# Kernel tuning notes

Hardware: AMD Instinct MI355X
Metric: run time of the kernel (lower is better)

Reference implementation:

```python
import jax, jax.numpy as jnp
import numpy as np


def gcn_layer(x, src, dst, deg_inv_sqrt, W, b):
    # PyG GCNConv: h = X W; out[i] = sum_{j->i} norm(j,i) * h[j] + deg_i^{-1} * h[i] + b
    n = x.shape[0]
    h = x @ W                                   # [N, out]
    norm = deg_inv_sqrt[src] * deg_inv_sqrt[dst]  # [E]
    msg = h[src] * norm[:, None]                # [E, out]
    agg = jax.ops.segment_sum(msg, dst, num_segments=n)
    # self-loop contribution (added loops with norm = deg_i^{-1})
    agg = agg + h * (deg_inv_sqrt * deg_inv_sqrt)[:, None]
    return agg + b


def setup_inputs() -> dict:
    key = jax.random.key(0)
    k1, k2, k3, k4, k5, k6 = jax.random.split(key, 6)
    N, E, IN, HID, OUT = 50000, 800000, 128, 128, 64
    x = jax.random.normal(k1, (N, IN), dtype=jnp.float32)
    edge_index = jax.random.randint(k2, (2, E), 0, N, dtype=jnp.int64)
    # glorot-ish init for weights, zeros-ish bias
    W1 = jax.random.normal(k3, (IN, HID), dtype=jnp.float32) * (1.0 / np.sqrt(IN))
    b1 = jax.random.normal(k4, (HID,), dtype=jnp.float32) * 0.01
    W2 = jax.random.normal(k5, (HID, OUT), dtype=jnp.float32) * (1.0 / np.sqrt(HID))
    b2 = jax.random.normal(k6, (OUT,), dtype=jnp.float32) * 0.01
    return {"x": x, "edge_index": edge_index, "W1": W1, "b1": b1, "W2": W2, "b2": b2}


def reference(x, edge_index, W1, b1, W2, b2):
    n = x.shape[0]
    src, dst = edge_index[0], edge_index[1]
    # degree with self-loops (PyG computes degree on the dst/col index)
    deg = jax.ops.segment_sum(jnp.ones_like(dst, dtype=x.dtype), dst, num_segments=n) + 1.0
    deg_inv_sqrt = jax.lax.rsqrt(deg)
    h = gcn_layer(x, src, dst, deg_inv_sqrt, W1, b1)
    h = jax.nn.relu(h)
    # F.dropout with training=False is identity (module evaluated in eval mode)
    out = gcn_layer(h, src, dst, deg_inv_sqrt, W2, b2)
    return out
```

## Files before the change

kernel.cpp:

```cpp
#include <hip/hip_runtime.h>
#include <stdint.h>

typedef __attribute__((ext_vector_type(8))) short short8;
typedef __attribute__((ext_vector_type(4))) float floatx4;

static inline size_t align256(size_t x) { return (x + 255) & ~size_t(255); }

__device__ __forceinline__ unsigned short f2bf(float f) {
    unsigned u = __float_as_uint(f);
    u += 0x7fff + ((u >> 16) & 1);
    return (unsigned short)(u >> 16);
}
__device__ __forceinline__ unsigned pack_bf16(float a, float b) {
    return (unsigned)f2bf(a) | ((unsigned)f2bf(b) << 16);
}
__device__ __forceinline__ float bf_lo(unsigned u) { return __uint_as_float(u << 16); }
__device__ __forceinline__ float bf_hi(unsigned u) { return __uint_as_float(u & 0xffff0000u); }

#define BSHIFT 7
#define NBMAX 1024
#define CH 2048
#define SCAP 3072

__device__ __forceinline__ bool detect_i32(const void* eidx, int E, int t) {
    const long long* e64 = (const long long*)eidx;
    int nchk = E < 256 ? E : 256;
    long long v = e64[t % nchk];
    int bad = (v < 0 || v > 0x7fffffffLL) ? 1 : 0;
    return __syncthreads_or(bad) != 0;
}

__global__ __launch_bounds__(256) void k_hist(const void* __restrict__ eidx, int E,
        int* __restrict__ chist, int NB, int NC,
        const float* __restrict__ W1, const float* __restrict__ W2,
        unsigned short* __restrict__ w1t, unsigned short* __restrict__ w2t,
        int K1, int M1, int K2, int M2) {
    __shared__ int hist[NBMAX];
    const int t = threadIdx.x, B = blockIdx.x;
    if (B < NC) {
        const int e0 = B * CH;
        const int e1 = (e0 + CH < E) ? e0 + CH : E;
        const bool i32 = detect_i32(eidx, E, t);
        const int* e32 = (const int*)eidx;
        const long long* e64 = (const long long*)eidx;
        for (int b0 = 0; b0 < NB; b0 += NBMAX) {
            int bw = (NB - b0 < NBMAX) ? NB - b0 : NBMAX;
            for (int i = t; i < bw; i += 256) hist[i] = 0;
            __syncthreads();
            for (int e = e0 + t; e < e1; e += 256) {
                int d = i32 ? e32[(size_t)E + e] : (int)e64[(size_t)E + e];
                int b = (d >> BSHIFT) - b0;
                if (b >= 0 && b < bw) atomicAdd(&hist[b], 1);
            }
            __syncthreads();
            for (int i = t; i < bw; i += 256) chist[(size_t)(b0 + i) * NC + B] = hist[i];
            __syncthreads();
        }
    } else if (B == NC) {
        for (int j = t; j < K1 * M1; j += 256) {
            int k = j / M1, n = j % M1;
            w1t[(size_t)n * K1 + k] = f2bf(W1[j]);
        }
    } else if (B == NC + 1) {
        for (int j = t; j < K2 * M2; j += 256) {
            int k = j / M2, n = j % M2;
            w2t[(size_t)n * K2 + k] = f2bf(W2[j]);
        }
    }
}

__global__ __launch_bounds__(256) void k_btot(const int* __restrict__ chist,
                                              int* __restrict__ btot, int NB, int NC) {
    int b = blockIdx.x * 4 + (threadIdx.x >> 6);
    if (b >= NB) return;
    int lane = threadIdx.x & 63;
    const int* row = chist + (size_t)b * NC;
    int v = 0;
    for (int i = lane; i < NC; i += 64) v += row[i];
    #pragma unroll
    for (int off = 32; off >= 1; off >>= 1) v += __shfl_xor(v, off, 64);
    if (lane == 0) btot[b] = v;
}

__global__ __launch_bounds__(1024) void k_bscan(const int* __restrict__ btot,
                                                int* __restrict__ bbase,
                                                int* __restrict__ rs_final,
                                                int NB, int N) {
    __shared__ int swt[16];
    const int t = threadIdx.x, lane = t & 63, w = t >> 6;
    int carry = 0;
    for (int base = 0; base < NB; base += 1024) {
        int i = base + t;
        int v = (i < NB) ? btot[i] : 0;
        int incl = v;
        #pragma unroll
        for (int off = 1; off < 64; off <<= 1) {
            int nbr = __shfl_up(incl, off, 64);
            if (lane >= off) incl += nbr;
        }
        if (lane == 63) swt[w] = incl;
        __syncthreads();
        int woff = 0;
        for (int j = 0; j < w; ++j) woff += swt[j];
        if (i < NB) bbase[i] = carry + woff + incl - v;
        int tot = 0;
        for (int j = 0; j < 16; ++j) tot += swt[j];
        carry += tot;
        __syncthreads();
    }
    if (t == 0) { bbase[NB] = carry; rs_final[N] = carry; }
}

__global__ __launch_bounds__(256) void k_hscan2(int* __restrict__ chist,
                                                const int* __restrict__ bbase,
                                                int NB, int NC) {
    int b = blockIdx.x * 4 + (threadIdx.x >> 6);
    if (b >= NB) return;
    int lane = threadIdx.x & 63;
    int* row = chist + (size_t)b * NC;
    int carry = bbase[b];
    for (int base = 0; base < NC; base += 64) {
        int i = base + lane;
        int v = (i < NC) ? row[i] : 0;
        int incl = v;
        #pragma unroll
        for (int off = 1; off < 64; off <<= 1) {
            int nbr = __shfl_up(incl, off, 64);
            if (lane >= off) incl += nbr;
        }
        if (i < NC) row[i] = carry + incl - v;
        carry += __shfl(incl, 63, 64);
    }
}

__global__ __launch_bounds__(256) void k_bfill(const void* __restrict__ eidx, int E,
                                               const int* __restrict__ chist,
                                               unsigned* __restrict__ bbuf, int NB, int NC) {
    __shared__ int rank[NBMAX];
    __shared__ int base[NBMAX];
    const int t = threadIdx.x, c = blockIdx.x;
    const int e0 = c * CH;
    const int e1 = (e0 + CH < E) ? e0 + CH : E;
    const bool i32 = detect_i32(eidx, E, t);
    const int* e32 = (const int*)eidx;
    const long long* e64 = (const long long*)eidx;
    for (int b0 = 0; b0 < NB; b0 += NBMAX) {
        int bw = (NB - b0 < NBMAX) ? NB - b0 : NBMAX;
        for (int i = t; i < bw; i += 256) {
            rank[i] = 0;
            base[i] = chist[(size_t)(b0 + i) * NC + c];
        }
        __syncthreads();
        for (int e = e0 + t; e < e1; e += 256) {
            int s, d;
            if (i32) { s = e32[e]; d = e32[(size_t)E + e]; }
            else     { s = (int)e64[e]; d = (int)e64[(size_t)E + e]; }
            int b = (d >> BSHIFT) - b0;
            if (b >= 0 && b < bw) {
                int slot = base[b] + atomicAdd(&rank[b], 1);
                bbuf[slot] = ((unsigned)(d & 127) << 25) | (unsigned)s;
            }
        }
        __syncthreads();
    }
}

__global__ __launch_bounds__(256) void k_sort(const unsigned* __restrict__ bbuf,
                                              const int* __restrict__ bbase,
                                              int* __restrict__ rs_final,
                                              float* __restrict__ dinv,
                                              int* __restrict__ esrc, int N) {
    __shared__ int hist[128];
    __shared__ int off[128];
    __shared__ int srcbuf[SCAP];
    const int b = blockIdx.x, t = threadIdx.x;
    const int node0 = b << BSHIFT;
    const int nloc = (N - node0 < 128) ? N - node0 : 128;
    const int s0 = bbase[b], s1 = bbase[b + 1];
    const int cnt = s1 - s0;
    if (t < 128) hist[t] = 0;
    __syncthreads();
    for (int i = s0 + t; i < s1; i += 256)
        atomicAdd(&hist[bbuf[i] >> 25], 1);
    __syncthreads();
    if (t < 64) {
        int carry = 0;
        #pragma unroll
        for (int base = 0; base < 128; base += 64) {
            int v = hist[base + t];
            int incl = v;
            #pragma unroll
            for (int o = 1; o < 64; o <<= 1) {
                int nbr = __shfl_up(incl, o, 64);
                if (t >= o) incl += nbr;
            }
            off[base + t] = carry + incl - v;
            carry += __shfl(incl, 63, 64);
        }
    }
    __syncthreads();
    if (t < nloc) {
        rs_final[node0 + t] = s0 + off[t];
        dinv[node0 + t] = rsqrtf((float)hist[t] + 1.0f);
    }
    __syncthreads();
    if (t < 128) hist[t] = 0;
    __syncthreads();
    if (cnt <= SCAP) {
        for (int i = s0 + t; i < s1; i += 256) {
            unsigned sd = bbuf[i];
            int lo = sd >> 25;
            int r = atomicAdd(&hist[lo], 1);
            srcbuf[off[lo] + r] = (int)(sd & 0x1ffffffu);
        }
        __syncthreads();
        for (int i = t; i < cnt; i += 256) esrc[s0 + i] = srcbuf[i];
    } else {
        for (int i = s0 + t; i < s1; i += 256) {
            unsigned sd = bbuf[i];
            int lo = sd >> 25;
            int r = atomicAdd(&hist[lo], 1);
            esrc[s0 + off[lo] + r] = (int)(sd & 0x1ffffffu);
        }
    }
}

template<int BN, bool AF32>
__global__ __launch_bounds__(256, 3) void k_gemm(
        const void* __restrict__ Av, const unsigned short* __restrict__ Bt,
        const float* __restrict__ dinv, unsigned short* __restrict__ C,
        int N, int M) {
    constexpr int LD = 136;
    __shared__ unsigned short As[64 * LD];
    __shared__ unsigned short Bs[BN * LD];
    const int tid = threadIdx.x;
    const int wave = tid >> 6, lane = tid & 63;
    const int q = lane >> 4, tm = lane & 15;
    const int row0 = blockIdx.x * 64;

    {
        const uint4* Bg = (const uint4*)Bt;
        #pragma unroll
        for (int it = 0; it < BN / 16; ++it) {
            int i = tid + it * 256;
            int r = i >> 4, o = i & 15;
            *(uint4*)&Bs[r * LD + o * 8] = Bg[(size_t)r * 16 + o];
        }
    }
    if (AF32) {
        const float4* Ag = (const float4*)Av;
        #pragma unroll
        for (int it = 0; it < 8; ++it) {
            int i = tid + it * 256;
            int r = i >> 5, o = i & 31;
            int row = row0 + r;
            float4 v = make_float4(0.f, 0.f, 0.f, 0.f);
            if (row < N) v = Ag[(size_t)row * 32 + o];
            uint2 pk;
            pk.x = pack_bf16(v.x, v.y);
            pk.y = pack_bf16(v.z, v.w);
            *(uint2*)&As[r * LD + o * 4] = pk;
        }
    } else {
        const uint4* Ag = (const uint4*)Av;
        #pragma unroll
        for (int it = 0; it < 4; ++it) {
            int i = tid + it * 256;
            int r = i >> 4, o = i & 15;
            int row = row0 + r;
            uint4 v = make_uint4(0, 0, 0, 0);
            if (row < N) v = Ag[(size_t)row * 16 + o];
            *(uint4*)&As[r * LD + o * 8] = v;
        }
    }
    __syncthreads();

    constexpr int NG = BN / 16;
    floatx4 acc[NG];
    #pragma unroll
    for (int g = 0; g < NG; ++g) acc[g] = (floatx4){0.f, 0.f, 0.f, 0.f};

    const int arow = wave * 16 + tm;
    #pragma unroll
    for (int kc = 0; kc < 4; ++kc) {
        short8 af = *(const short8*)&As[arow * LD + kc * 32 + q * 8];
        #pragma unroll
        for (int g = 0; g < NG; ++g) {
            short8 bf = *(const short8*)&Bs[(g * 16 + tm) * LD + kc * 32 + q * 8];
            acc[g] = __builtin_amdgcn_mfma_f32_16x16x32_bf16(af, bf, acc[g], 0, 0, 0);
        }
    }

    float dv[4];
    #pragma unroll
    for (int r = 0; r < 4; ++r) {
        int row = row0 + wave * 16 + q * 4 + r;
        dv[r] = (row < N) ? dinv[row] : 0.f;
    }
    #pragma unroll
    for (int g = 0; g < NG; ++g) {
        #pragma unroll
        for (int r = 0; r < 4; ++r) {
            int row = row0 + wave * 16 + q * 4 + r;
            if (row < N) C[(size_t)row * M + g * 16 + tm] = f2bf(dv[r] * acc[g][r]);
        }
    }
}

#define ACC8(v) do { \
    a0 += bf_lo((v).x); a1 += bf_hi((v).x); \
    a2 += bf_lo((v).y); a3 += bf_hi((v).y); \
    a4 += bf_lo((v).z); a5 += bf_hi((v).z); \
    a6 += bf_lo((v).w); a7 += bf_hi((v).w); } while (0)

__global__ __launch_bounds__(256) void k_agg128(const uint4* __restrict__ H4,
        const float* __restrict__ dinv, const int* __restrict__ rs,
        const int* __restrict__ esrc, const float* __restrict__ bias,
        uint4* __restrict__ out, int N) {
    int wid = (blockIdx.x * 256 + threadIdx.x) >> 6;
    if (wid >= N) return;
    int l = threadIdx.x & 63;
    int g = l >> 4;
    int q = l & 15;
    float a0 = 0.f, a1 = 0.f, a2 = 0.f, a3 = 0.f;
    float a4 = 0.f, a5 = 0.f, a6 = 0.f, a7 = 0.f;
    int k0 = rs[wid], kend = rs[wid + 1];
    for (int base = k0; base < kend; base += 64) {
        int rem = kend - base; if (rem > 64) rem = 64;
        int idx = esrc[base + (l < rem ? l : 0)];
        int e0 = 0;
        for (; e0 + 16 <= rem; e0 += 16) {
            int s0 = __shfl(idx, e0 + g, 64);
            int s1 = __shfl(idx, e0 + 4 + g, 64);
            int s2 = __shfl(idx, e0 + 8 + g, 64);
            int s3 = __shfl(idx, e0 + 12 + g, 64);
            uint4 v0 = H4[(size_t)s0 * 16 + q];
            uint4 v1 = H4[(size_t)s1 * 16 + q];
            uint4 v2 = H4[(size_t)s2 * 16 + q];
            uint4 v3 = H4[(size_t)s3 * 16 + q];
            ACC8(v0); ACC8(v1); ACC8(v2); ACC8(v3);
        }
        for (; e0 + 4 <= rem; e0 += 4) {
            int s0 = __shfl(idx, e0 + g, 64);
            uint4 v0 = H4[(size_t)s0 * 16 + q];
            ACC8(v0);
        }
        if (e0 < rem) {
            int s0 = __shfl(idx, e0 + g, 64);
            if (e0 + g < rem) {
                uint4 v0 = H4[(size_t)s0 * 16 + q];
                ACC8(v0);
            }
        }
    }
    a0 += __shfl_xor(a0, 16, 64); a1 += __shfl_xor(a1, 16, 64);
    a2 += __shfl_xor(a2, 16, 64); a3 += __shfl_xor(a3, 16, 64);
    a4 += __shfl_xor(a4, 16, 64); a5 += __shfl_xor(a5, 16, 64);
    a6 += __shfl_xor(a6, 16, 64); a7 += __shfl_xor(a7, 16, 64);
    a0 += __shfl_xor(a0, 32, 64); a1 += __shfl_xor(a1, 32, 64);
    a2 += __shfl_xor(a2, 32, 64); a3 += __shfl_xor(a3, 32, 64);
    a4 += __shfl_xor(a4, 32, 64); a5 += __shfl_xor(a5, 32, 64);
    a6 += __shfl_xor(a6, 32, 64); a7 += __shfl_xor(a7, 32, 64);
    if (g == 0) {
        uint4 sv = H4[(size_t)wid * 16 + q];
        ACC8(sv);
        float di = dinv[wid];
        float4 bA = ((const float4*)bias)[q * 2];
        float4 bB = ((const float4*)bias)[q * 2 + 1];
        float o0 = fmaxf(fmaf(di, a0, bA.x), 0.f);
        float o1 = fmaxf(fmaf(di, a1, bA.y), 0.f);
        float o2 = fmaxf(fmaf(di, a2, bA.z), 0.f);
        float o3 = fmaxf(fmaf(di, a3, bA.w), 0.f);
        float o4 = fmaxf(fmaf(di, a4, bB.x), 0.f);
        float o5 = fmaxf(fmaf(di, a5, bB.y), 0.f);
        float o6 = fmaxf(fmaf(di, a6, bB.z), 0.f);
        float o7 = fmaxf(fmaf(di, a7, bB.w), 0.f);
        uint4 pk;
        pk.x = pack_bf16(o0, o1);
        pk.y = pack_bf16(o2, o3);
        pk.z = pack_bf16(o4, o5);
        pk.w = pack_bf16(o6, o7);
        out[(size_t)wid * 16 + q] = pk;
    }
}

__global__ __launch_bounds__(256) void k_agg64(const uint4* __restrict__ H4,
        const float* __restrict__ dinv, const int* __restrict__ rs,
        const int* __restrict__ esrc, const float* __restrict__ bias,
        float4* __restrict__ out, int N) {
    int wid = (blockIdx.x * 256 + threadIdx.x) >> 6;
    if (wid >= N) return;
    int l = threadIdx.x & 63;
    int g = l >> 3;
    int q = l & 7;
    float a0 = 0.f, a1 = 0.f, a2 = 0.f, a3 = 0.f;
    float a4 = 0.f, a5 = 0.f, a6 = 0.f, a7 = 0.f;
    int k0 = rs[wid], kend = rs[wid + 1];
    for (int base = k0; base < kend; base += 64) {
        int rem = kend - base; if (rem > 64) rem = 64;
        int idx = esrc[base + (l < rem ? l : 0)];
        int e0 = 0;
        for (; e0 + 32 <= rem; e0 += 32) {
            int s0 = __shfl(idx, e0 + g, 64);
            int s1 = __shfl(idx, e0 + 8 + g, 64);
            int s2 = __shfl(idx, e0 + 16 + g, 64);
            int s3 = __shfl(idx, e0 + 24 + g, 64);
            uint4 v0 = H4[(size_t)s0 * 8 + q];
            uint4 v1 = H4[(size_t)s1 * 8 + q];
            uint4 v2 = H4[(size_t)s2 * 8 + q];
            uint4 v3 = H4[(size_t)s3 * 8 + q];
            ACC8(v0); ACC8(v1); ACC8(v2); ACC8(v3);
        }
        for (; e0 + 8 <= rem; e0 += 8) {
            int s0 = __shfl(idx, e0 + g, 64);
            uint4 v0 = H4[(size_t)s0 * 8 + q];
            ACC8(v0);
        }
        if (e0 < rem) {
            int s0 = __shfl(idx, e0 + g, 64);
            if (e0 + g < rem) {
                uint4 v0 = H4[(size_t)s0 * 8 + q];
                ACC8(v0);
            }
        }
    }
    a0 += __shfl_xor(a0, 8, 64);  a1 += __shfl_xor(a1, 8, 64);
    a2 += __shfl_xor(a2, 8, 64);  a3 += __shfl_xor(a3, 8, 64);
    a4 += __shfl_xor(a4, 8, 64);  a5 += __shfl_xor(a5, 8, 64);
    a6 += __shfl_xor(a6, 8, 64);  a7 += __shfl_xor(a7, 8, 64);
    a0 += __shfl_xor(a0, 16, 64); a1 += __shfl_xor(a1, 16, 64);
    a2 += __shfl_xor(a2, 16, 64); a3 += __shfl_xor(a3, 16, 64);
    a4 += __shfl_xor(a4, 16, 64); a5 += __shfl_xor(a5, 16, 64);
    a6 += __shfl_xor(a6, 16, 64); a7 += __shfl_xor(a7, 16, 64);
    a0 += __shfl_xor(a0, 32, 64); a1 += __shfl_xor(a1, 32, 64);
    a2 += __shfl_xor(a2, 32, 64); a3 += __shfl_xor(a3, 32, 64);
    a4 += __shfl_xor(a4, 32, 64); a5 += __shfl_xor(a5, 32, 64);
    a6 += __shfl_xor(a6, 32, 64); a7 += __shfl_xor(a7, 32, 64);
    if (g == 0) {
        uint4 sv = H4[(size_t)wid * 8 + q];
        ACC8(sv);
        float di = dinv[wid];
        float4 bA = ((const float4*)bias)[q * 2];
        float4 bB = ((const float4*)bias)[q * 2 + 1];
        float4 oA, oB;
        oA.x = fmaf(di, a0, bA.x);
        oA.y = fmaf(di, a1, bA.y);
        oA.z = fmaf(di, a2, bA.z);
        oA.w = fmaf(di, a3, bA.w);
        oB.x = fmaf(di, a4, bB.x);
        oB.y = fmaf(di, a5, bB.y);
        oB.z = fmaf(di, a6, bB.z);
        oB.w = fmaf(di, a7, bB.w);
        out[(size_t)wid * 16 + q * 2]     = oA;
        out[(size_t)wid * 16 + q * 2 + 1] = oB;
    }
}

extern "C" void kernel_launch(void* const* d_in, const int* in_sizes, int n_in,
                              void* d_out, int out_size, void* d_ws, size_t ws_size,
                              hipStream_t stream) {
    const float* x  = (const float*)d_in[0];
    const void*  ei = d_in[1];
    const float* W1 = (const float*)d_in[2];
    const float* b1 = (const float*)d_in[3];
    const float* W2 = (const float*)d_in[4];
    const float* b2 = (const float*)d_in[5];

    int HID = in_sizes[3];
    int IN  = in_sizes[2] / HID;
    int OUT = in_sizes[4] / HID;
    int N   = in_sizes[0] / IN;
    int E   = in_sizes[1] / 2;
    int NB  = (N + 127) >> BSHIFT;
    int NC  = (E + CH - 1) / CH;

    char* p = (char*)d_ws;
    int* chist     = (int*)p;   p += align256((size_t)NB * NC * 4);
    int* btot      = (int*)p;   p += align256((size_t)NB * 4);
    int* bbase     = (int*)p;   p += align256((size_t)(NB + 1) * 4);
    int* rs_final  = (int*)p;   p += align256((size_t)(N + 1) * 4);
    int* esrc      = (int*)p;   p += align256((size_t)E * 4);
    float* dinv    = (float*)p; p += align256((size_t)N * 4);
    unsigned short* w1t = (unsigned short*)p; p += align256((size_t)HID * IN * 2);
    unsigned short* w2t = (unsigned short*)p; p += align256((size_t)OUT * HID * 2);
    size_t hb_bytes = (size_t)N * HID * 2, bbuf_bytes = (size_t)E * 4;
    unsigned* bbuf = (unsigned*)p;
    unsigned short* hb = (unsigned short*)p;
    p += align256(hb_bytes > bbuf_bytes ? hb_bytes : bbuf_bytes);
    unsigned short* h1b = (unsigned short*)p; p += align256((size_t)N * HID * 2);
    unsigned short* h2b = (unsigned short*)p; p += align256((size_t)N * OUT * 2);

    k_hist<<<NC + 2, 256, 0, stream>>>(ei, E, chist, NB, NC,
                                       W1, W2, w1t, w2t, IN, HID, HID, OUT);
    k_btot<<<(NB + 3) / 4, 256, 0, stream>>>(chist, btot, NB, NC);
    k_bscan<<<1, 1024, 0, stream>>>(btot, bbase, rs_final, NB, N);
    k_hscan2<<<(NB + 3) / 4, 256, 0, stream>>>(chist, bbase, NB, NC);
    k_bfill<<<NC, 256, 0, stream>>>(ei, E, chist, bbuf, NB, NC);
    k_sort<<<NB, 256, 0, stream>>>(bbuf, bbase, rs_final, dinv, esrc, N);

    k_gemm<128, true><<<(N + 63) / 64, 256, 0, stream>>>(x, w1t, dinv, hb, N, HID);
    k_agg128<<<(N + 3) / 4, 256, 0, stream>>>((const uint4*)hb, dinv, rs_final, esrc,
                                              b1, (uint4*)h1b, N);

    k_gemm<64, false><<<(N + 63) / 64, 256, 0, stream>>>(h1b, w2t, dinv, h2b, N, OUT);
    k_agg64<<<(N + 3) / 4, 256, 0, stream>>>((const uint4*)h2b, dinv, rs_final, esrc,
                                             b2, (float4*)d_out, N);
}
```

Measured before the change: 201.4 us.

## Sort edges within each destination by source-range bucket for gather locality

The per-block counting sort now keys on destination-low bits combined with 6 bits of source index (a 13-bit key, 8192 bins), so edges for each destination are grouped by coarse source range. The aim is better cache locality in the later gather of h[src] during aggregation. In exchange the sort kernel zeroes and scans a 32KB shared histogram per block, which raises its own cost and shared-memory footprint and may reduce occupancy.

```diff
diff --git a/kernel.cpp b/kernel.cpp
--- a/kernel.cpp
+++ b/kernel.cpp
@@ -21,6 +21,7 @@
 #define NBMAX 1024
 #define CH 2048
 #define SCAP 3072
+#define KB 8192
 
 __device__ __forceinline__ bool detect_i32(const void* eidx, int E, int t) {
     const long long* e64 = (const long long*)eidx;
@@ -28,6 +29,24 @@
     long long v = e64[t % nchk];
     int bad = (v < 0 || v > 0x7fffffffLL) ? 1 : 0;
     return __syncthreads_or(bad) != 0;
+}
+
+__device__ __forceinline__ int blockScanExcl(int v, int t, int* sw, int* tot) {
+    int lane = t & 63, w = t >> 6;
+    int incl = v;
+    #pragma unroll
+    for (int off = 1; off < 64; off <<= 1) {
+        int nbr = __shfl_up(incl, off, 64);
+        if (lane >= off) incl += nbr;
+    }
+    if (lane == 63) sw[w] = incl;
+    __syncthreads();
+    int woff = 0;
+    for (int j = 0; j < w; ++j) woff += sw[j];
+    int tt = sw[0] + sw[1] + sw[2] + sw[3];
+    __syncthreads();
+    *tot = tt;
+    return woff + incl - v;
 }
 
 __global__ __launch_bounds__(256) void k_hist(const void* __restrict__ eidx, int E,
@@ -165,62 +184,68 @@
     }
 }
 
-__global__ __launch_bounds__(256) void k_sort(const unsigned* __restrict__ bbuf,
-                                              const int* __restrict__ bbase,
-                                              int* __restrict__ rs_final,
-                                              float* __restrict__ dinv,
-                                              int* __restrict__ esrc, int N) {
-    __shared__ int hist[128];
-    __shared__ int off[128];
+__global__ __launch_bounds__(256, 3) void k_sort(const unsigned* __restrict__ bbuf,
+                                                 const int* __restrict__ bbase,
+                                                 int* __restrict__ rs_final,
+                                                 float* __restrict__ dinv,
+                                                 int* __restrict__ esrc, int N) {
+    __shared__ int h13[KB];
     __shared__ int srcbuf[SCAP];
+    __shared__ int sw[4];
     const int b = blockIdx.x, t = threadIdx.x;
     const int node0 = b << BSHIFT;
     const int nloc = (N - node0 < 128) ? N - node0 : 128;
     const int s0 = bbase[b], s1 = bbase[b + 1];
     const int cnt = s1 - s0;
-    if (t < 128) hist[t] = 0;
-    __syncthreads();
-    for (int i = s0 + t; i < s1; i += 256)
-        atomicAdd(&hist[bbuf[i] >> 25], 1);
-    __syncthreads();
-    if (t < 64) {
-        int carry = 0;
-        #pragma unroll
-        for (int base = 0; base < 128; base += 64) {
-            int v = hist[base + t];
-            int incl = v;
-            #pragma unroll
-            for (int o = 1; o < 64; o <<= 1) {
-                int nbr = __shfl_up(incl, o, 64);
-                if (t >= o) incl += nbr;
-            }
-            off[base + t] = carry + incl - v;
-            carry += __shfl(incl, 63, 64);
+    #pragma unroll
+    for (int j = 0; j < KB / 256; ++j) h13[t + j * 256] = 0;
+    __syncthreads();
+    for (int i = s0 + t; i < s1; i += 256) {
+        unsigned u = bbuf[i];
+        unsigned src = u & 0x1ffffffu;
+        int key = (int)((u >> 25) << 6) | (int)((src >> 11) & 63u);
+        atomicAdd(&h13[key], 1);
+    }
+    __syncthreads();
+    {
+        const int CPT = KB / 256;
+        int s = 0;
+        #pragma unroll
+        for (int j = 0; j < CPT; ++j) s += h13[t * CPT + j];
+        int tot;
+        int run = blockScanExcl(s, t, sw, &tot);
+        #pragma unroll
+        for (int j = 0; j < CPT; ++j) {
+            int v = h13[t * CPT + j];
+            h13[t * CPT + j] = run;
+            run += v;
         }
     }
     __syncthreads();
     if (t < nloc) {
-        rs_final[node0 + t] = s0 + off[t];
-        dinv[node0 + t] = rsqrtf((float)hist[t] + 1.0f);
-    }
-    __syncthreads();
-    if (t < 128) hist[t] = 0;
+        int st = h13[t << 6];
+        int en = (t < 127) ? h13[(t + 1) << 6] : cnt;
+        rs_final[node0 + t] = s0 + st;
+        dinv[node0 + t] = rsqrtf((float)(en - st) + 1.0f);
+    }
     __syncthreads();
     if (cnt <= SCAP) {
         for (int i = s0 + t; i < s1; i += 256) {
-            unsigned sd = bbuf[i];
-            int lo = sd >> 25;
-            int r = atomicAdd(&hist[lo], 1);
-            srcbuf[off[lo] + r] = (int)(sd & 0x1ffffffu);
+            unsigned u = bbuf[i];
+            unsigned src = u & 0x1ffffffu;
+            int key = (int)((u >> 25) << 6) | (int)((src >> 11) & 63u);
+            int slot = atomicAdd(&h13[key], 1);
+            srcbuf[slot] = (int)src;
         }
         __syncthreads();
         for (int i = t; i < cnt; i += 256) esrc[s0 + i] = srcbuf[i];
     } else {
         for (int i = s0 + t; i < s1; i += 256) {
-            unsigned sd = bbuf[i];
-            int lo = sd >> 25;
-            int r = atomicAdd(&hist[lo], 1);
-            esrc[s0 + off[lo] + r] = (int)(sd & 0x1ffffffu);
+            unsigned u = bbuf[i];
+            unsigned src = u & 0x1ffffffu;
+            int key = (int)((u >> 25) << 6) | (int)((src >> 11) & 63u);
+            int slot = atomicAdd(&h13[key], 1);
+            esrc[s0 + slot] = (int)src;
         }
     }
 }
```

After: 205.7 us. 2.1% more time.

## Replace per-chunk histogram scans with global atomic cursors in bucket fill

Applied to the files above, without the earlier changes.

The bucketing pipeline drops the per-chunk column histogram and its two-level scan. A single scan kernel now sums a small fixed-chunk histogram to get bucket bases and cursors. Fill blocks recount their own edges and reserve slots with one global atomicAdd per bucket. This removes two kernel launches and a large chist matrix, at the cost of reading dst twice in bk_fill, making edge order within a bucket nondeterministic, and assuming NB fits in shared memory (NBMAX).

```diff
diff --git a/kernel.cpp b/kernel.cpp
--- a/kernel.cpp
+++ b/kernel.cpp
@@ -19,7 +19,8 @@
 
 #define BSHIFT 7
 #define NBMAX 1024
-#define CH 2048
+#define NHC 64
+#define NCF 128
 #define SCAP 3072
 
 __device__ __forceinline__ bool detect_i32(const void* eidx, int E, int t) {
@@ -31,37 +32,33 @@
 }
 
 __global__ __launch_bounds__(256) void k_hist(const void* __restrict__ eidx, int E,
-        int* __restrict__ chist, int NB, int NC,
+        int* __restrict__ chist, int NB,
         const float* __restrict__ W1, const float* __restrict__ W2,
         unsigned short* __restrict__ w1t, unsigned short* __restrict__ w2t,
         int K1, int M1, int K2, int M2) {
     __shared__ int hist[NBMAX];
     const int t = threadIdx.x, B = blockIdx.x;
-    if (B < NC) {
-        const int e0 = B * CH;
-        const int e1 = (e0 + CH < E) ? e0 + CH : E;
+    if (B < NHC) {
+        const int ehc = (E + NHC - 1) / NHC;
+        const int e0 = B * ehc;
+        const int e1 = (e0 + ehc < E) ? e0 + ehc : E;
         const bool i32 = detect_i32(eidx, E, t);
         const int* e32 = (const int*)eidx;
         const long long* e64 = (const long long*)eidx;
-        for (int b0 = 0; b0 < NB; b0 += NBMAX) {
-            int bw = (NB - b0 < NBMAX) ? NB - b0 : NBMAX;
-            for (int i = t; i < bw; i += 256) hist[i] = 0;
-            __syncthreads();
-            for (int e = e0 + t; e < e1; e += 256) {
-                int d = i32 ? e32[(size_t)E + e] : (int)e64[(size_t)E + e];
-                int b = (d >> BSHIFT) - b0;
-                if (b >= 0 && b < bw) atomicAdd(&hist[b], 1);
-            }
-            __syncthreads();
-            for (int i = t; i < bw; i += 256) chist[(size_t)(b0 + i) * NC + B] = hist[i];
-            __syncthreads();
-        }
-    } else if (B == NC) {
+        for (int i = t; i < NB; i += 256) hist[i] = 0;
+        __syncthreads();
+        for (int e = e0 + t; e < e1; e += 256) {
+            int d = i32 ? e32[(size_t)E + e] : (int)e64[(size_t)E + e];
+            atomicAdd(&hist[d >> BSHIFT], 1);
+        }
+        __syncthreads();
+        for (int i = t; i < NB; i += 256) chist[(size_t)i * NHC + B] = hist[i];
+    } else if (B == NHC) {
         for (int j = t; j < K1 * M1; j += 256) {
             int k = j / M1, n = j % M1;
             w1t[(size_t)n * K1 + k] = f2bf(W1[j]);
         }
-    } else if (B == NC + 1) {
+    } else if (B == NHC + 1) {
         for (int j = t; j < K2 * M2; j += 256) {
             int k = j / M2, n = j % M2;
             w2t[(size_t)n * K2 + k] = f2bf(W2[j]);
@@ -69,29 +66,23 @@
     }
 }
 
-__global__ __launch_bounds__(256) void k_btot(const int* __restrict__ chist,
-                                              int* __restrict__ btot, int NB, int NC) {
-    int b = blockIdx.x * 4 + (threadIdx.x >> 6);
-    if (b >= NB) return;
-    int lane = threadIdx.x & 63;
-    const int* row = chist + (size_t)b * NC;
-    int v = 0;
-    for (int i = lane; i < NC; i += 64) v += row[i];
-    #pragma unroll
-    for (int off = 32; off >= 1; off >>= 1) v += __shfl_xor(v, off, 64);
-    if (lane == 0) btot[b] = v;
-}
-
-__global__ __launch_bounds__(1024) void k_bscan(const int* __restrict__ btot,
-                                                int* __restrict__ bbase,
-                                                int* __restrict__ rs_final,
-                                                int NB, int N) {
+__global__ __launch_bounds__(1024) void k_scan1(const int* __restrict__ chist,
+        int* __restrict__ bbase, int* __restrict__ cursor,
+        int* __restrict__ rs_final, int NB, int N) {
     __shared__ int swt[16];
     const int t = threadIdx.x, lane = t & 63, w = t >> 6;
     int carry = 0;
     for (int base = 0; base < NB; base += 1024) {
         int i = base + t;
-        int v = (i < NB) ? btot[i] : 0;
+        int v = 0;
+        if (i < NB) {
+            const int4* row = (const int4*)(chist + (size_t)i * NHC);
+            #pragma unroll
+            for (int c = 0; c < NHC / 4; ++c) {
+                int4 q = row[c];
+                v += q.x + q.y + q.z + q.w;
+            }
+        }
         int incl = v;
         #pragma unroll
         for (int off = 1; off < 64; off <<= 1) {
@@ -102,7 +93,11 @@
         __syncthreads();
         int woff = 0;
         for (int j = 0; j < w; ++j) woff += swt[j];
-        if (i < NB) bbase[i] = carry + woff + incl - v;
+        if (i < NB) {
+            int ex = carry + woff + incl - v;
+            bbase[i] = ex;
+            cursor[i] = ex;
+        }
         int tot = 0;
         for (int j = 0; j < 16; ++j) tot += swt[j];
         carry += tot;
@@ -111,57 +106,39 @@
     if (t == 0) { bbase[NB] = carry; rs_final[N] = carry; }
 }
 
-__global__ __launch_bounds__(256) void k_hscan2(int* __restrict__ chist,
-                                                const int* __restrict__ bbase,
-                                                int NB, int NC) {
-    int b = blockIdx.x * 4 + (threadIdx.x >> 6);
-    if (b >= NB) return;
-    int lane = threadIdx.x & 63;
-    int* row = chist + (size_t)b * NC;
-    int carry = bbase[b];
-    for (int base = 0; base < NC; base += 64) {
-        int i = base + lane;
-        int v = (i < NC) ? row[i] : 0;
-        int incl = v;
-        #pragma unroll
-        for (int off = 1; off < 64; off <<= 1) {
-            int nbr = __shfl_up(incl, off, 64);
-            if (lane >= off) incl += nbr;
-        }
-        if (i < NC) row[i] = carry + incl - v;
-        carry += __shfl(incl, 63, 64);
-    }
-}
-
 __global__ __launch_bounds__(256) void k_bfill(const void* __restrict__ eidx, int E,
-                                               const int* __restrict__ chist,
-                                               unsigned* __restrict__ bbuf, int NB, int NC) {
+                                               int* __restrict__ cursor,
+                                               unsigned* __restrict__ bbuf, int NB) {
     __shared__ int rank[NBMAX];
     __shared__ int base[NBMAX];
-    const int t = threadIdx.x, c = blockIdx.x;
-    const int e0 = c * CH;
-    const int e1 = (e0 + CH < E) ? e0 + CH : E;
+    const int t = threadIdx.x, B = blockIdx.x;
+    const int ecf = (E + NCF - 1) / NCF;
+    const int e0 = B * ecf;
+    const int e1 = (e0 + ecf < E) ? e0 + ecf : E;
     const bool i32 = detect_i32(eidx, E, t);
     const int* e32 = (const int*)eidx;
     const long long* e64 = (const long long*)eidx;
-    for (int b0 = 0; b0 < NB; b0 += NBMAX) {
-        int bw = (NB - b0 < NBMAX) ? NB - b0 : NBMAX;
-        for (int i = t; i < bw; i += 256) {
-            rank[i] = 0;
-            base[i] = chist[(size_t)(b0 + i) * NC + c];
-        }
-        __syncthreads();
-        for (int e = e0 + t; e < e1; e += 256) {
-            int s, d;
-            if (i32) { s = e32[e]; d = e32[(size_t)E + e]; }
-            else     { s = (int)e64[e]; d = (int)e64[(size_t)E + e]; }
-            int b = (d >> BSHIFT) - b0;
-            if (b >= 0 && b < bw) {
-                int slot = base[b] + atomicAdd(&rank[b], 1);
-                bbuf[slot] = ((unsigned)(d & 127) << 25) | (unsigned)s;
-            }
-        }
-        __syncthreads();
+    for (int i = t; i < NB; i += 256) rank[i] = 0;
+    __syncthreads();
+    for (int e = e0 + t; e < e1; e += 256) {
+        int d = i32 ? e32[(size_t)E + e] : (int)e64[(size_t)E + e];
+        atomicAdd(&rank[d >> BSHIFT], 1);
+    }
+    __syncthreads();
+    for (int i = t; i < NB; i += 256) {
+        int c = rank[i];
+        base[i] = c ? atomicAdd(&cursor[i], c) : 0;
+    }
+    __syncthreads();
+    for (int i = t; i < NB; i += 256) rank[i] = 0;
+    __syncthreads();
+    for (int e = e0 + t; e < e1; e += 256) {
+        int s, d;
+        if (i32) { s = e32[e]; d = e32[(size_t)E + e]; }
+        else     { s = (int)e64[e]; d = (int)e64[(size_t)E + e]; }
+        int b = d >> BSHIFT;
+        int slot = base[b] + atomicAdd(&rank[b], 1);
+        bbuf[slot] = ((unsigned)(d & 127) << 25) | (unsigned)s;
     }
 }
 
@@ -472,12 +449,11 @@
     int N   = in_sizes[0] / IN;
     int E   = in_sizes[1] / 2;
     int NB  = (N + 127) >> BSHIFT;
-    int NC  = (E + CH - 1) / CH;
 
     char* p = (char*)d_ws;
-    int* chist     = (int*)p;   p += align256((size_t)NB * NC * 4);
-    int* btot      = (int*)p;   p += align256((size_t)NB * 4);
+    int* chist     = (int*)p;   p += align256((size_t)NB * NHC * 4);
     int* bbase     = (int*)p;   p += align256((size_t)(NB + 1) * 4);
+    int* cursor    = (int*)p;   p += align256((size_t)NB * 4);
     int* rs_final  = (int*)p;   p += align256((size_t)(N + 1) * 4);
     int* esrc      = (int*)p;   p += align256((size_t)E * 4);
     float* dinv    = (float*)p; p += align256((size_t)N * 4);
@@ -490,12 +466,10 @@
     unsigned short* h1b = (unsigned short*)p; p += align256((size_t)N * HID * 2);
     unsigned short* h2b = (unsigned short*)p; p += align256((size_t)N * OUT * 2);
 
-    k_hist<<<NC + 2, 256, 0, stream>>>(ei, E, chist, NB, NC,
-                                       W1, W2, w1t, w2t, IN, HID, HID, OUT);
-    k_btot<<<(NB + 3) / 4, 256, 0, stream>>>(chist, btot, NB, NC);
-    k_bscan<<<1, 1024, 0, stream>>>(btot, bbase, rs_final, NB, N);
-    k_hscan2<<<(NB + 3) / 4, 256, 0, stream>>>(chist, bbase, NB, NC);
-    k_bfill<<<NC, 256, 0, stream>>>(ei, E, chist, bbuf, NB, NC);
+    k_hist<<<NHC + 2, 256, 0, stream>>>(ei, E, chist, NB,
+                                        W1, W2, w1t, w2t, IN, HID, HID, OUT);
+    k_scan1<<<1, 1024, 0, stream>>>(chist, bbase, cursor, rs_final, NB, N);
+    k_bfill<<<NCF, 256, 0, stream>>>(ei, E, cursor, bbuf, NB);
     k_sort<<<NB, 256, 0, stream>>>(bbuf, bbase, rs_final, dinv, esrc, N);
 
     k_gemm<128, true><<<(N + 63) / 64, 256, 0, stream>>>(x, w1t, dinv, hb, N, HID);
```

Measured after the change: 215.7 us. +7.1%, slower.
